# Optimization experiments

Hardware: AMD Instinct MI355X
Metric: run time of the kernel (lower is better)

## Reference

```python
import jax, jax.numpy as jnp
import numpy as np

B, STATE_DIM, HIDDEN, ACTION_DIM = 262144, 128, 256, 8


def setup_inputs() -> dict:
    key = jax.random.key(0)
    ks = jax.random.split(key, 5)
    state = jax.random.normal(ks[0], (B, STATE_DIM), dtype=jnp.float32)
    # torch init: weight.data.normal_(0, 0.01); biases left at default -> zeros here
    W1 = jax.random.normal(ks[1], (HIDDEN, STATE_DIM), dtype=jnp.float32) * 0.01
    b1 = jnp.zeros((HIDDEN,), dtype=jnp.float32)
    W2 = jax.random.normal(ks[2], (HIDDEN, HIDDEN), dtype=jnp.float32) * 0.01
    b2 = jnp.zeros((HIDDEN,), dtype=jnp.float32)
    W3 = jax.random.normal(ks[3], (2 * ACTION_DIM, HIDDEN), dtype=jnp.float32) * 0.01
    b3 = jnp.zeros((2 * ACTION_DIM,), dtype=jnp.float32)
    # reparameterized noise for torch.normal(u, s): sample = u + |s| * eps
    eps = jax.random.normal(ks[4], (B, ACTION_DIM), dtype=jnp.float32)
    return {"state": state, "W1": W1, "b1": b1, "W2": W2, "b2": b2,
            "W3": W3, "b3": b3, "eps": eps}


def reference(state, W1, b1, W2, b2, W3, b3, eps):
    x = state.reshape(-1, STATE_DIM)
    h = jax.nn.relu(x @ W1.T + b1)
    h = jax.nn.relu(h @ W2.T + b2)
    n = h @ W3.T + b3                       # [B, 2*ACTION_DIM]
    u = n[:, :ACTION_DIM]                   # mean
    s = jnp.abs(n[:, ACTION_DIM:])          # std (abs as in np.abs)
    action = jax.nn.sigmoid(u + s * eps)    # sigmoid(normal(u, s))
    return (action * 8 + 1).astype(jnp.int32)  # (action*8+1).int(), per row
```

## Files before the change

kernel.cpp:

```cpp
#include <hip/hip_runtime.h>
#include <math.h>

#define NB  262144
#define SD  128
#define HID 256
#define AD  8

typedef float v2f __attribute__((ext_vector_type(2)));

#define W1T_OFF 0
#define W2T_OFF (SD*HID)
#define W3P_OFF (W2T_OFF + HID*HID)
#define B1_OFF  (W3P_OFF + HID*2*AD)
#define B2_OFF  (B1_OFF + HID)
#define B3P_OFF (B2_OFF + HID)
#define WS_FLOATS (B3P_OFF + 2*AD)

__global__ __launch_bounds__(256) void prep_weights(
    const float* __restrict__ W1, const float* __restrict__ b1,
    const float* __restrict__ W2, const float* __restrict__ b2,
    const float* __restrict__ W3, const float* __restrict__ b3,
    float* __restrict__ ws) {
  int stride = gridDim.x * blockDim.x;
  for (int i = blockIdx.x * blockDim.x + threadIdx.x; i < WS_FLOATS; i += stride) {
    float v;
    if (i < W2T_OFF) {
      int k = i >> 8, j = i & 255;
      v = W1[j * SD + k];
    } else if (i < W3P_OFF) {
      int t = i - W2T_OFF;
      int k = t >> 8, j = t & 255;
      v = W2[j * HID + k];
    } else if (i < B1_OFF) {
      int t = i - W3P_OFF;
      int k = t >> 4, a = (t >> 1) & 7, h = t & 1;
      v = W3[(a + 8 * h) * HID + k];
    } else if (i < B2_OFF) {
      v = b1[i - B1_OFF];
    } else if (i < B3P_OFF) {
      v = b2[i - B2_OFF];
    } else {
      int t = i - B3P_OFF;
      v = b3[(t >> 1) + 8 * (t & 1)];
    }
    ws[i] = v;
  }
}


__global__ __launch_bounds__(256, 3) void actor_fused(
    const float* __restrict__ state, const float* __restrict__ eps,
    const float* __restrict__ ws, int* __restrict__ out) {
  __shared__ float s_h[32][264];

  const int tid  = threadIdx.x;
  const int lane = tid & 63;
  const int wvu  = __builtin_amdgcn_readfirstlane(tid >> 6);
  const long wrow = (long)blockIdx.x * 32 + wvu * 8;

  const float4* __restrict__ W1T4 = (const float4*)(ws + W1T_OFF);
  const float4* __restrict__ W2T4 = (const float4*)(ws + W2T_OFF);
  const v2f*    __restrict__ W3P  = (const v2f*)(ws + W3P_OFF);

  const float* __restrict__ xbase = state + wrow * SD;

  float acc[8][4];
  #pragma unroll
  for (int r = 0; r < 8; ++r)
    #pragma unroll
    for (int c = 0; c < 4; ++c) acc[r][c] = 0.0f;

  #pragma unroll 2
  for (int k0 = 0; k0 < SD; k0 += 4) {
    float4 w[4];
    #pragma unroll
    for (int j = 0; j < 4; ++j) w[j] = W1T4[(k0 + j) * 64 + lane];
    float4 xv[8];
    #pragma unroll
    for (int r = 0; r < 8; ++r)
      xv[r] = *(const float4*)(xbase + r * SD + k0);
    #pragma unroll
    for (int j = 0; j < 4; ++j) {
      #pragma unroll
      for (int r = 0; r < 8; ++r) {
        float x = (j == 0) ? xv[r].x : (j == 1) ? xv[r].y
                : (j == 2) ? xv[r].z : xv[r].w;
        acc[r][0] = fmaf(x, w[j].x, acc[r][0]);
        acc[r][1] = fmaf(x, w[j].y, acc[r][1]);
        acc[r][2] = fmaf(x, w[j].z, acc[r][2]);
        acc[r][3] = fmaf(x, w[j].w, acc[r][3]);
      }
    }
  }

  {
    float4 bb = ((const float4*)(ws + B1_OFF))[lane];
    #pragma unroll
    for (int r = 0; r < 8; ++r) {
      float4 hv;
      hv.x = acc[r][0] + bb.x; hv.y = acc[r][1] + bb.y;
      hv.z = acc[r][2] + bb.z; hv.w = acc[r][3] + bb.w;
      hv.x = hv.x > 0.0f ? hv.x : 0.0f;
      hv.y = hv.y > 0.0f ? hv.y : 0.0f;
      hv.z = hv.z > 0.0f ? hv.z : 0.0f;
      hv.w = hv.w > 0.0f ? hv.w : 0.0f;
      *(float4*)&s_h[wvu * 8 + r][4 * lane] = hv;
    }
  }

  #pragma unroll
  for (int r = 0; r < 8; ++r)
    #pragma unroll
    for (int c = 0; c < 4; ++c) acc[r][c] = 0.0f;

  #pragma unroll 2
  for (int k0 = 0; k0 < HID; k0 += 4) {
    float4 w[4];
    #pragma unroll
    for (int j = 0; j < 4; ++j) w[j] = W2T4[(k0 + j) * 64 + lane];
    float4 xv[8];
    #pragma unroll
    for (int r = 0; r < 8; ++r)
      xv[r] = *(const float4*)&s_h[wvu * 8 + r][k0];
    #pragma unroll
    for (int j = 0; j < 4; ++j) {
      #pragma unroll
      for (int r = 0; r < 8; ++r) {
        float x = (j == 0) ? xv[r].x : (j == 1) ? xv[r].y
                : (j == 2) ? xv[r].z : xv[r].w;
        acc[r][0] = fmaf(x, w[j].x, acc[r][0]);
        acc[r][1] = fmaf(x, w[j].y, acc[r][1]);
        acc[r][2] = fmaf(x, w[j].z, acc[r][2]);
        acc[r][3] = fmaf(x, w[j].w, acc[r][3]);
      }
    }
  }

  {
    float4 bb = ((const float4*)(ws + B2_OFF))[lane];
    #pragma unroll
    for (int r = 0; r < 8; ++r) {
      float4 hv;
      hv.x = acc[r][0] + bb.x; hv.y = acc[r][1] + bb.y;
      hv.z = acc[r][2] + bb.z; hv.w = acc[r][3] + bb.w;
      hv.x = hv.x > 0.0f ? hv.x : 0.0f;
      hv.y = hv.y > 0.0f ? hv.y : 0.0f;
      hv.z = hv.z > 0.0f ? hv.z : 0.0f;
      hv.w = hv.w > 0.0f ? hv.w : 0.0f;
      *(float4*)&s_h[wvu * 8 + r][4 * lane] = hv;
    }
  }

  {
    const int r3 = lane >> 3;
    const int a  = lane & 7;
    const float* __restrict__ h2row = &s_h[wvu * 8 + r3][0];
    float accu = 0.0f, accs = 0.0f;
    #pragma unroll 2
    for (int k0 = 0; k0 < HID; k0 += 4) {
      v2f ha = *(const v2f*)(h2row + k0);
      v2f hb = *(const v2f*)(h2row + k0 + 2);
      v2f wp0 = W3P[(k0 + 0) * 8 + a];
      v2f wp1 = W3P[(k0 + 1) * 8 + a];
      v2f wp2 = W3P[(k0 + 2) * 8 + a];
      v2f wp3 = W3P[(k0 + 3) * 8 + a];
      accu = fmaf(ha.x, wp0.x, accu); accs = fmaf(ha.x, wp0.y, accs);
      accu = fmaf(ha.y, wp1.x, accu); accs = fmaf(ha.y, wp1.y, accs);
      accu = fmaf(hb.x, wp2.x, accu); accs = fmaf(hb.x, wp2.y, accs);
      accu = fmaf(hb.y, wp3.x, accu); accs = fmaf(hb.y, wp3.y, accs);
    }
    v2f b3p = ((const v2f*)(ws + B3P_OFF))[a];
    float nu = accu + b3p.x;
    float ns = accs + b3p.y;

    long grow = wrow + r3;
    float sa = fabsf(ns);
    float ev = eps[grow * AD + a];
    float t  = __fmul_rn(sa, ev);
    float z  = __fadd_rn(nu, t);
    float e  = (float)exp(-(double)z);
    float d  = __fadd_rn(1.0f, e);
    float act = 1.0f / d;
    float q  = act * 8.0f;
    float wq = __fadd_rn(q, 1.0f);
    out[grow * AD + a] = (int)wq;
  }
}

extern "C" void kernel_launch(void* const* d_in, const int* in_sizes, int n_in,
                              void* d_out, int out_size, void* d_ws, size_t ws_size,
                              hipStream_t stream) {
  const float* state = (const float*)d_in[0];
  const float* W1    = (const float*)d_in[1];
  const float* b1    = (const float*)d_in[2];
  const float* W2    = (const float*)d_in[3];
  const float* b2    = (const float*)d_in[4];
  const float* W3    = (const float*)d_in[5];
  const float* b3    = (const float*)d_in[6];
  const float* eps   = (const float*)d_in[7];
  int*   out = (int*)d_out;
  float* ws  = (float*)d_ws;

  hipLaunchKernelGGL(prep_weights, dim3(128), dim3(256), 0, stream,
                     W1, b1, W2, b2, W3, b3, ws);
  hipLaunchKernelGGL(actor_fused, dim3(NB / 32), dim3(256), 0, stream,
                     state, eps, ws, out);
}
```

Before: 877.1 us.

## Stage input rows in LDS, prefetch weights one step ahead, raise occupancy

Each wave now copies its 8 input rows into shared memory with coalesced loads up front, then reads layer-1 activations from LDS instead of doing strided global float4 loads. Both GEMM loops double-buffer the weight loads, fetching the next k-step's weights while computing the current one. The eps value is loaded at kernel start, and launch bounds rise to 4 blocks per SM. The aim is to hide global latency and improve coalescing, at the cost of extra registers for the prefetch buffers under a tighter register budget.

Result: slower. 1.759 ms (+100.6%).

```diff
diff --git a/kernel.cpp b/kernel.cpp
--- a/kernel.cpp
+++ b/kernel.cpp
@@ -47,8 +47,7 @@
   }
 }
 
-
-__global__ __launch_bounds__(256, 3) void actor_fused(
+__global__ __launch_bounds__(256, 4) void actor_fused(
     const float* __restrict__ state, const float* __restrict__ eps,
     const float* __restrict__ ws, int* __restrict__ out) {
   __shared__ float s_h[32][264];
@@ -62,7 +61,13 @@
   const float4* __restrict__ W2T4 = (const float4*)(ws + W2T_OFF);
   const v2f*    __restrict__ W3P  = (const v2f*)(ws + W3P_OFF);
 
-  const float* __restrict__ xbase = state + wrow * SD;
+  const float epsv = eps[wrow * AD + lane];
+
+  #pragma unroll
+  for (int r = 0; r < 8; ++r) {
+    v2f xr = *(const v2f*)(state + (wrow + r) * SD + 2 * lane);
+    *(v2f*)&s_h[wvu * 8 + r][2 * lane] = xr;
+  }
 
   float acc[8][4];
   #pragma unroll
@@ -70,26 +75,33 @@
     #pragma unroll
     for (int c = 0; c < 4; ++c) acc[r][c] = 0.0f;
 
-  #pragma unroll 2
-  for (int k0 = 0; k0 < SD; k0 += 4) {
-    float4 w[4];
-    #pragma unroll
-    for (int j = 0; j < 4; ++j) w[j] = W1T4[(k0 + j) * 64 + lane];
-    float4 xv[8];
-    #pragma unroll
-    for (int r = 0; r < 8; ++r)
-      xv[r] = *(const float4*)(xbase + r * SD + k0);
-    #pragma unroll
-    for (int j = 0; j < 4; ++j) {
-      #pragma unroll
-      for (int r = 0; r < 8; ++r) {
-        float x = (j == 0) ? xv[r].x : (j == 1) ? xv[r].y
-                : (j == 2) ? xv[r].z : xv[r].w;
-        acc[r][0] = fmaf(x, w[j].x, acc[r][0]);
-        acc[r][1] = fmaf(x, w[j].y, acc[r][1]);
-        acc[r][2] = fmaf(x, w[j].z, acc[r][2]);
-        acc[r][3] = fmaf(x, w[j].w, acc[r][3]);
+  {
+    float4 w[4], wn[4];
+    #pragma unroll
+    for (int j = 0; j < 4; ++j) w[j] = W1T4[j * 64 + lane];
+    #pragma unroll 2
+    for (int k0 = 0; k0 < SD; k0 += 4) {
+      const int kn = (k0 + 4) & (SD - 1);
+      #pragma unroll
+      for (int j = 0; j < 4; ++j) wn[j] = W1T4[(kn + j) * 64 + lane];
+      float4 xv[8];
+      #pragma unroll
+      for (int r = 0; r < 8; ++r)
+        xv[r] = *(const float4*)&s_h[wvu * 8 + r][k0];
+      #pragma unroll
+      for (int j = 0; j < 4; ++j) {
+        #pragma unroll
+        for (int r = 0; r < 8; ++r) {
+          float x = (j == 0) ? xv[r].x : (j == 1) ? xv[r].y
+                  : (j == 2) ? xv[r].z : xv[r].w;
+          acc[r][0] = fmaf(x, w[j].x, acc[r][0]);
+          acc[r][1] = fmaf(x, w[j].y, acc[r][1]);
+          acc[r][2] = fmaf(x, w[j].z, acc[r][2]);
+          acc[r][3] = fmaf(x, w[j].w, acc[r][3]);
+        }
       }
+      #pragma unroll
+      for (int j = 0; j < 4; ++j) w[j] = wn[j];
     }
   }
 
@@ -113,26 +125,33 @@
     #pragma unroll
     for (int c = 0; c < 4; ++c) acc[r][c] = 0.0f;
 
-  #pragma unroll 2
-  for (int k0 = 0; k0 < HID; k0 += 4) {
-    float4 w[4];
-    #pragma unroll
-    for (int j = 0; j < 4; ++j) w[j] = W2T4[(k0 + j) * 64 + lane];
-    float4 xv[8];
-    #pragma unroll
-    for (int r = 0; r < 8; ++r)
-      xv[r] = *(const float4*)&s_h[wvu * 8 + r][k0];
-    #pragma unroll
-    for (int j = 0; j < 4; ++j) {
-      #pragma unroll
-      for (int r = 0; r < 8; ++r) {
-        float x = (j == 0) ? xv[r].x : (j == 1) ? xv[r].y
-                : (j == 2) ? xv[r].z : xv[r].w;
-        acc[r][0] = fmaf(x, w[j].x, acc[r][0]);
-        acc[r][1] = fmaf(x, w[j].y, acc[r][1]);
-        acc[r][2] = fmaf(x, w[j].z, acc[r][2]);
-        acc[r][3] = fmaf(x, w[j].w, acc[r][3]);
+  {
+    float4 w[4], wn[4];
+    #pragma unroll
+    for (int j = 0; j < 4; ++j) w[j] = W2T4[j * 64 + lane];
+    #pragma unroll 2
+    for (int k0 = 0; k0 < HID; k0 += 4) {
+      const int kn = (k0 + 4) & (HID - 1);
+      #pragma unroll
+      for (int j = 0; j < 4; ++j) wn[j] = W2T4[(kn + j) * 64 + lane];
+      float4 xv[8];
+      #pragma unroll
+      for (int r = 0; r < 8; ++r)
+        xv[r] = *(const float4*)&s_h[wvu * 8 + r][k0];
+      #pragma unroll
+      for (int j = 0; j < 4; ++j) {
+        #pragma unroll
+        for (int r = 0; r < 8; ++r) {
+          float x = (j == 0) ? xv[r].x : (j == 1) ? xv[r].y
+                  : (j == 2) ? xv[r].z : xv[r].w;
+          acc[r][0] = fmaf(x, w[j].x, acc[r][0]);
+          acc[r][1] = fmaf(x, w[j].y, acc[r][1]);
+          acc[r][2] = fmaf(x, w[j].z, acc[r][2]);
+          acc[r][3] = fmaf(x, w[j].w, acc[r][3]);
+        }
       }
+      #pragma unroll
+      for (int j = 0; j < 4; ++j) w[j] = wn[j];
     }
   }
 
@@ -175,8 +194,7 @@
 
     long grow = wrow + r3;
     float sa = fabsf(ns);
-    float ev = eps[grow * AD + a];
-    float t  = __fmul_rn(sa, ev);
+    float t  = __fmul_rn(sa, epsv);
     float z  = __fadd_rn(nu, t);
     float e  = (float)exp(-(double)z);
     float d  = __fadd_rn(1.0f, e);
```
